# Kernel optimization log

Hardware: AMD Instinct MI355X
Metric: run time of the kernel (lower is better)

The kernel has to match this reference:

```python
import jax, jax.numpy as jnp
import numpy as np

N_PTS = 131072
IN_CH = 63
IN_CH_VIEWS = 27
WIDTH = 256
NUM_HEADS = 4
SCALE = 0.05


def setup_inputs() -> dict:
    key = jax.random.key(0)
    ks = jax.random.split(key, 12)
    H, W = NUM_HEADS, WIDTH
    inp = {
        'x': jax.random.normal(ks[0], (N_PTS, IN_CH + IN_CH_VIEWS), jnp.float32),
        'head_idx': jax.random.randint(ks[1], (N_PTS,), 0, NUM_HEADS),
        # shared trunk: layer0 63->256, layers1..3 256->256 (no skip before split_at=4)
        'W0': jax.random.normal(ks[2], (IN_CH, W), jnp.float32) * SCALE,
        'b0': jnp.zeros((W,), jnp.float32),
        'Ws': jax.random.normal(ks[3], (3, W, W), jnp.float32) * SCALE,
        'bs': jnp.zeros((3, W), jnp.float32),
        # per-head tails: g=4 in skips -> (W+63)->W, then g=5..7 W->W
        'tW0': jax.random.normal(ks[4], (H, W + IN_CH, W), jnp.float32) * SCALE,
        'tb0': jnp.zeros((H, W), jnp.float32),
        'tWs': jax.random.normal(ks[5], (H, 3, W, W), jnp.float32) * SCALE,
        'tbs': jnp.zeros((H, 3, W), jnp.float32),
        # per-head viewdirs output heads
        'featW': jax.random.normal(ks[6], (H, W, W), jnp.float32) * SCALE,
        'featb': jnp.zeros((H, W), jnp.float32),
        'alphaW': jax.random.normal(ks[7], (H, W, 1), jnp.float32) * SCALE,
        'alphab': jnp.zeros((H, 1), jnp.float32),
        'viewsW': jax.random.normal(ks[8], (H, IN_CH_VIEWS + W, W // 2), jnp.float32) * SCALE,
        'viewsb': jnp.zeros((H, W // 2), jnp.float32),
        'rgbW': jax.random.normal(ks[9], (H, W // 2, 3), jnp.float32) * SCALE,
        'rgbb': jnp.zeros((H, 3), jnp.float32),
    }
    return inp


def reference(x, head_idx, W0, b0, Ws, bs, tW0, tb0, tWs, tbs,
              featW, featb, alphaW, alphab, viewsW, viewsb, rgbW, rgbb):
    input_pts = x[:, :IN_CH]          # [N, 63]
    input_views = x[:, IN_CH:]        # [N, 27]

    # shared trunk (layers 0..3, no skip hits in this range)
    h = jax.nn.relu(input_pts @ W0 + b0)
    for i in range(Ws.shape[0]):
        h = jax.nn.relu(h @ Ws[i] + bs[i])

    # per-head tails, computed densely for ALL heads (as in the original)
    # first tail layer g=4 is a skip layer: concat input_pts
    ht = jnp.concatenate([input_pts, h], axis=-1)          # [N, 319]
    ha = jax.nn.relu(jnp.einsum('nf,hfo->nho', ht, tW0) + tb0[None])  # [N, H, 256]
    for j in range(tWs.shape[1]):
        ha = jax.nn.relu(jnp.einsum('nho,hop->nhp', ha, tWs[:, j]) + tbs[None, :, j])

    # per-head viewdir output heads
    alpha = jnp.einsum('nho,hop->nhp', ha, alphaW) + alphab[None]     # [N, H, 1]
    feat = jnp.einsum('nho,hop->nhp', ha, featW) + featb[None]        # [N, H, 256]
    views_b = jnp.broadcast_to(input_views[:, None, :], (x.shape[0], feat.shape[1], IN_CH_VIEWS))
    hv = jnp.concatenate([feat, views_b], axis=-1)                    # [N, H, 283]
    hv = jax.nn.relu(jnp.einsum('nho,hop->nhp', hv, viewsW) + viewsb[None])
    rgb = jnp.einsum('nho,hop->nhp', hv, rgbW) + rgbb[None]           # [N, H, 3]

    outs = jnp.concatenate([rgb, alpha], axis=-1)                     # [N, H, 4]
    sel = jnp.take_along_axis(outs, head_idx[:, None, None], axis=1)[:, 0]  # [N, 4]
    return sel
```

## Files before the change

kernel.cpp:

```cpp
#include <hip/hip_runtime.h>

#define N_PTS 131072
#define TILE 64
#define THREADS 256
#define REGION 40960

typedef __bf16 bf16;
typedef __bf16 bf16x8 __attribute__((ext_vector_type(8)));
typedef float f32x4 __attribute__((ext_vector_type(4)));

#define WS_PERM_OFF   256
#define WS_WPACK_OFF  (256 + 4 * REGION * 4)
#define OFF_W0     0
#define OFF_WS     16384
#define OFF_TW0    212992
#define OFF_TWS    540672
#define OFF_FEATW  1327104
#define OFF_VIEWSW 1589248
#define TOTAL_PACK 1736704

#define H_BASE 0
#define B_BASE 32768
#define LDS_BYTES 81920

__device__ __forceinline__ unsigned swz(unsigned base, unsigned row, unsigned rowstride,
                                        unsigned kbyte) {
  return (base + row * rowstride + kbyte) ^ ((row & 7u) << 4);
}

__device__ __forceinline__ void gload_lds16(const bf16* g, char* l) {
  __builtin_amdgcn_global_load_lds(
      (const __attribute__((address_space(1))) void*)g,
      (__attribute__((address_space(3))) void*)l, 16, 0, 0);
}

template <int N>
__device__ __forceinline__ void wait_vm() {
  asm volatile("s_waitcnt vmcnt(%0)" ::"n"(N) : "memory");
}

__global__ void k_pack(const float* __restrict__ W0, const float* __restrict__ Ws,
                       const float* __restrict__ tW0, const float* __restrict__ tWs,
                       const float* __restrict__ featW, const float* __restrict__ viewsW,
                       bf16* __restrict__ out, const int* __restrict__ head,
                       int* __restrict__ ctrl, int* __restrict__ perm) {
  int gid = blockIdx.x * blockDim.x + threadIdx.x;
  if (gid < N_PTS) {
    int h = head[gid];
    int lane = threadIdx.x & 63;
    #pragma unroll
    for (int hh = 0; hh < 4; ++hh) {
      unsigned long long m = __ballot(h == hh);
      if (m == 0ull) continue;
      int leader = __builtin_ctzll(m);
      int base = 0;
      if (lane == leader) base = atomicAdd(&ctrl[16 + hh], __popcll(m));
      base = __shfl(base, leader);
      if (h == hh) {
        int rank = __popcll(m & ((1ull << lane) - 1ull));
        perm[hh * REGION + base + rank] = gid;
      }
    }
  }

  for (int idx = gid; idx < TOTAL_PACK; idx += gridDim.x * blockDim.x) {
    float v; int dst;
    if (idx < 16384) {
      int k = idx >> 8, o = idx & 255;
      v = (k < 63) ? W0[k * 256 + o] : 0.f;
      dst = OFF_W0 + o * 64 + k;
    } else if (idx < 212992) {
      int i = idx - 16384; int l = i >> 16, r = i & 65535, k = r >> 8, o = r & 255;
      v = Ws[i];
      dst = OFF_WS + l * 65536 + o * 256 + k;
    } else if (idx < 540672) {
      int i = idx - 212992; int h = i / 81920, r = i % 81920, k = r >> 8, o = r & 255;
      v = (k < 63) ? tW0[(h * 319 + k) * 256 + o]
                   : (k == 63 ? 0.f : tW0[(h * 319 + k - 1) * 256 + o]);
      dst = OFF_TW0 + h * 81920 + o * 320 + k;
    } else if (idx < 1327104) {
      int i = idx - 540672; int hj = i >> 16, r = i & 65535, k = r >> 8, o = r & 255;
      v = tWs[i];
      dst = OFF_TWS + hj * 65536 + o * 256 + k;
    } else if (idx < 1589248) {
      int i = idx - 1327104; int h = i >> 16, r = i & 65535, k = r >> 8, o = r & 255;
      v = featW[i];
      dst = OFF_FEATW + h * 65536 + o * 256 + k;
    } else {
      int i = idx - 1589248; int h = i / 36864, r = i % 36864, k = r >> 7, o = r & 127;
      v = (k < 283) ? viewsW[(h * 283 + k) * 128 + o] : 0.f;
      dst = OFF_VIEWSW + h * 36864 + o * 288 + k;
    }
    out[dst] = (bf16)v;
  }
}

template <int NF, bool RELU, int RKC, int LKC, bool REG_FIRST, int OUTS>
__device__ __forceinline__ void mfma_layer(char* lds, const bf16* __restrict__ Wt,
                                           int wK, const float* __restrict__ bias,
                                           const bf16x8* aregs, int lane, int wave) {
  const int l15 = lane & 15, l4 = lane >> 4;
  constexpr int KC = RKC + LKC;
  f32x4 acc[4][NF];
  #pragma unroll
  for (int m = 0; m < 4; ++m)
    #pragma unroll
    for (int n = 0; n < NF; ++n) acc[m][n] = (f32x4){0.f, 0.f, 0.f, 0.f};

  const int c0 = wave * (NF * 16);
  const int wbase = B_BASE + wave * 12288;

  float bv[NF];
  #pragma unroll
  for (int n = 0; n < NF; ++n) bv[n] = bias[c0 + n * 16 + l15];

  const int breg = wbase + l15 * 64 + ((l4 ^ ((l15 >> 1) & 3)) << 4);

  unsigned acur = (unsigned)(l15 * 512 + l4 * 16);
  const unsigned axor = (l15 & 7u) << 4;

  const bf16* gsrc[NF];
  #pragma unroll
  for (int s = 0; s < NF; ++s) {
    int op = s * 16 + (lane >> 2);
    int j = lane & 3;
    gsrc[s] = Wt + (c0 + op) * wK + ((j ^ ((op >> 1) & 3)) << 3);
  }

  #pragma unroll
  for (int s = 0; s < NF; ++s) { gload_lds16(gsrc[s], lds + wbase + s * 1024); gsrc[s] += 32; }
  #pragma unroll
  for (int s = 0; s < NF; ++s) { gload_lds16(gsrc[s], lds + wbase + 4096 + s * 1024); gsrc[s] += 32; }

  int rd = 0, st = 8192;

  auto dostep = [&](int kc, const bf16x8* ar) {
    if (kc + 2 < KC) {
      #pragma unroll
      for (int s = 0; s < NF; ++s) { gload_lds16(gsrc[s], lds + wbase + st + s * 1024); gsrc[s] += 32; }
      st = (st == 8192) ? 0 : st + 4096;
      wait_vm<2 * NF>();
    } else if (kc + 1 < KC) {
      wait_vm<NF>();
    } else {
      wait_vm<0>();
    }

    bf16x8 a[4];
    if (ar) {
      #pragma unroll
      for (int m = 0; m < 4; ++m) a[m] = ar[m];
    } else {
      unsigned va = acur ^ axor;
      #pragma unroll
      for (int m = 0; m < 4; ++m) a[m] = *(const bf16x8*)(lds + va + m * 8192);
      acur += 64;
    }
    bf16x8 b[NF];
    #pragma unroll
    for (int n = 0; n < NF; ++n) b[n] = *(const bf16x8*)(lds + breg + rd + n * 1024);
    rd = (rd == 8192) ? 0 : rd + 4096;

    __builtin_amdgcn_s_setprio(1);
    #pragma unroll
    for (int n = 0; n < NF; ++n)
      #pragma unroll
      for (int m = 0; m < 4; ++m)
        acc[m][n] = __builtin_amdgcn_mfma_f32_16x16x32_bf16(a[m], b[n], acc[m][n], 0, 0, 0);
    __builtin_amdgcn_s_setprio(0);
  };

  if constexpr (REG_FIRST && RKC >= 1) dostep(0, aregs);
  if constexpr (REG_FIRST && RKC >= 2) dostep(1, aregs + 4);
  #pragma unroll 1
  for (int kc = (REG_FIRST ? RKC : 0); kc < (REG_FIRST ? KC : LKC); ++kc)
    dostep(kc, nullptr);
  if constexpr (!REG_FIRST && RKC >= 1) dostep(KC - 1, aregs);

  __builtin_amdgcn_s_barrier();

  #pragma unroll
  for (int n = 0; n < NF; ++n) {
    int col = c0 + n * 16 + l15;
    #pragma unroll
    for (int m = 0; m < 4; ++m) {
      #pragma unroll
      for (int j = 0; j < 4; ++j) {
        float v = acc[m][n][j] + bv[n];
        if (RELU) v = fmaxf(v, 0.f);
        int row = m * 16 + l4 * 4 + j;
        *(bf16*)(lds + swz(H_BASE, row, 512, col * 2)) = (bf16)v;
      }
    }
  }
  __syncthreads();
}

__global__ __launch_bounds__(THREADS, 2) void k_main(
    const float* __restrict__ x, const int* __restrict__ ctrl, const int* __restrict__ perm,
    const bf16* __restrict__ wpack,
    const float* __restrict__ b0, const float* __restrict__ bs,
    const float* __restrict__ tb0p, const float* __restrict__ tbsp,
    const float* __restrict__ featb, const float* __restrict__ alphaW,
    const float* __restrict__ alphab, const float* __restrict__ viewsb,
    const float* __restrict__ rgbW, const float* __restrict__ rgbb,
    float* __restrict__ outp) {
  __shared__ __attribute__((aligned(16))) char lds[LDS_BYTES];

  const int tid = threadIdx.x;
  const int lane = tid & 63, wave = tid >> 6;
  const int l15 = lane & 15, l4 = lane >> 4;

  const int hh = blockIdx.x / (REGION / TILE);
  const int start = (blockIdx.x % (REGION / TILE)) * TILE;
  const int cnt = ctrl[16 + hh];
  if (start >= cnt) return;
  const int nv = min(TILE, cnt - start);
  const int permbase = hh * REGION + start;

  bf16x8 ptsreg[8];
  bf16x8 viewsreg[4];
  #pragma unroll
  for (int m = 0; m < 4; ++m) {
    int row = m * 16 + l15;
    bool valid = (start + row) < cnt;
    int p = valid ? perm[permbase + row] : 0;
    const float* xr = x + p * 90;
    #pragma unroll
    for (int rkc = 0; rkc < 2; ++rkc) {
      int k0 = rkc * 32 + l4 * 8;
      bf16x8 f;
      #pragma unroll
      for (int j = 0; j < 8; ++j) {
        int k = k0 + j;
        f[j] = (bf16)((valid && k < 63) ? xr[k] : 0.f);
      }
      ptsreg[rkc * 4 + m] = f;
    }
    {
      int k0 = l4 * 8;
      bf16x8 f;
      #pragma unroll
      for (int j = 0; j < 8; ++j) {
        int k = k0 + j;
        f[j] = (bf16)((valid && k < 27) ? xr[63 + k] : 0.f);
      }
      viewsreg[m] = f;
    }
  }

  const bf16* W0p    = wpack + OFF_W0;
  const bf16* Wsp    = wpack + OFF_WS;
  const bf16* tW0p   = wpack + OFF_TW0 + hh * 81920;
  const bf16* tWsp   = wpack + OFF_TWS + hh * 3 * 65536;
  const bf16* featWp = wpack + OFF_FEATW + hh * 65536;
  const bf16* viewsWp= wpack + OFF_VIEWSW + hh * 36864;

  mfma_layer<4, true, 2, 0, true,  256>(lds, W0p, 64, b0, ptsreg, lane, wave);
  mfma_layer<4, true, 0, 8, false, 256>(lds, Wsp,          256, bs,       nullptr, lane, wave);
  mfma_layer<4, true, 0, 8, false, 256>(lds, Wsp + 65536,  256, bs + 256, nullptr, lane, wave);
  mfma_layer<4, true, 0, 8, false, 256>(lds, Wsp + 131072, 256, bs + 512, nullptr, lane, wave);
  mfma_layer<4, true, 2, 8, true,  256>(lds, tW0p, 320, tb0p + hh * 256, ptsreg, lane, wave);

  mfma_layer<4, true, 0, 8, false, 256>(lds, tWsp,          256, tbsp + hh * 768,       nullptr, lane, wave);
  mfma_layer<4, true, 0, 8, false, 256>(lds, tWsp + 65536,  256, tbsp + hh * 768 + 256, nullptr, lane, wave);
  mfma_layer<4, true, 0, 8, false, 256>(lds, tWsp + 131072, 256, tbsp + hh * 768 + 512, nullptr, lane, wave);

  float my_alpha;
  {
    int p = wave * 16 + l15;
    int kq = lane >> 4;
    const float* aW = alphaW + hh * 256;
    float s = 0.f;
    for (int i = 0; i < 8; ++i) {
      int k = kq * 64 + i * 8;
      bf16x8 hv8 = *(const bf16x8*)(lds + swz(H_BASE, p, 512, k * 2));
      #pragma unroll
      for (int j = 0; j < 8; ++j) s += (float)hv8[j] * aW[k + j];
    }
    s += __shfl_xor(s, 16);
    s += __shfl_xor(s, 32);
    my_alpha = s + alphab[hh];
  }

  mfma_layer<4, false, 0, 8, false, 256>(lds, featWp, 256, featb + hh * 256, nullptr, lane, wave);
  mfma_layer<2, true, 1, 8, false, 128>(lds, viewsWp, 288, viewsb + hh * 128, viewsreg, lane, wave);

  {
    int p = wave * 16 + l15;
    int kq = lane >> 4;
    const float* rW = rgbW + hh * 128 * 3;
    float r0 = 0.f, r1 = 0.f, r2 = 0.f;
    for (int i = 0; i < 4; ++i) {
      int k = kq * 32 + i * 8;
      bf16x8 hv8 = *(const bf16x8*)(lds + swz(H_BASE, p, 512, k * 2));
      #pragma unroll
      for (int j = 0; j < 8; ++j) {
        float hvf = (float)hv8[j];
        r0 += hvf * rW[(k + j) * 3 + 0];
        r1 += hvf * rW[(k + j) * 3 + 1];
        r2 += hvf * rW[(k + j) * 3 + 2];
      }
    }
    r0 += __shfl_xor(r0, 16); r0 += __shfl_xor(r0, 32);
    r1 += __shfl_xor(r1, 16); r1 += __shfl_xor(r1, 32);
    r2 += __shfl_xor(r2, 16); r2 += __shfl_xor(r2, 32);
    if (kq == 0 && p < nv) {
      int pt = perm[permbase + p];
      float4 o = make_float4(r0 + rgbb[hh * 3 + 0], r1 + rgbb[hh * 3 + 1],
                             r2 + rgbb[hh * 3 + 2], my_alpha);
      *(float4*)(outp + pt * 4) = o;
    }
  }
}

extern "C" void kernel_launch(void* const* d_in, const int* in_sizes, int n_in,
                              void* d_out, int out_size, void* d_ws, size_t ws_size,
                              hipStream_t stream) {
  const float* x      = (const float*)d_in[0];
  const int*   head   = (const int*)d_in[1];
  const float* W0     = (const float*)d_in[2];
  const float* b0     = (const float*)d_in[3];
  const float* Ws     = (const float*)d_in[4];
  const float* bs     = (const float*)d_in[5];
  const float* tW0    = (const float*)d_in[6];
  const float* tb0    = (const float*)d_in[7];
  const float* tWs    = (const float*)d_in[8];
  const float* tbs    = (const float*)d_in[9];
  const float* featW  = (const float*)d_in[10];
  const float* featb  = (const float*)d_in[11];
  const float* alphaW = (const float*)d_in[12];
  const float* alphab = (const float*)d_in[13];
  const float* viewsW = (const float*)d_in[14];
  const float* viewsb = (const float*)d_in[15];
  const float* rgbW   = (const float*)d_in[16];
  const float* rgbb   = (const float*)d_in[17];

  int*  ctrl  = (int*)d_ws;
  int*  perm  = (int*)((char*)d_ws + WS_PERM_OFF);
  bf16* wpack = (bf16*)((char*)d_ws + WS_WPACK_OFF);

  hipMemsetAsync(ctrl, 0, 256, stream);
  k_pack<<<2048, 256, 0, stream>>>(W0, Ws, tW0, tWs, featW, viewsW, wpack, head, ctrl, perm);
  k_main<<<4 * (REGION / TILE), THREADS, 0, stream>>>(x, ctrl, perm, wpack,
                                                      b0, bs, tb0, tbs, featb, alphaW, alphab,
                                                      viewsb, rgbW, rgbb, (float*)d_out);
}
```

Before: 422.1 us.

## Prefetch next layer's weights across layers and stage inputs in LDS

The weight streaming drops from a three-slot ring to a double buffer. On its last K step each layer now issues the first weight chunk of the next layer, so the pipeline bubble at layer boundaries is hidden. The pts and views inputs are staged in swizzled LDS instead of per-thread registers, and the permutation indices are cached in LDS. This frees VGPRs and lowers total LDS use. In exchange, the shallower prefetch depth may expose global-load latency within each layer, and the kernel now relies on hand-placed waitcnt and barrier pairs for LDS correctness.

```diff
diff --git a/kernel.cpp b/kernel.cpp
--- a/kernel.cpp
+++ b/kernel.cpp
@@ -19,9 +19,12 @@
 #define OFF_VIEWSW 1589248
 #define TOTAL_PACK 1736704
 
-#define H_BASE 0
-#define B_BASE 32768
-#define LDS_BYTES 81920
+#define H_BASE     0
+#define PTS_BASE   32768
+#define VIEWS_BASE 40960
+#define PIDX_BASE  45056
+#define RING_BASE  46080
+#define LDS_BYTES  78848
 
 __device__ __forceinline__ unsigned swz(unsigned base, unsigned row, unsigned rowstride,
                                         unsigned kbyte) {
@@ -95,12 +98,14 @@
   }
 }
 
-template <int NF, bool RELU, int RKC, int LKC, bool REG_FIRST, int OUTS>
+template <int NF, bool RELU, int PKC, int LKC, bool PTS_FIRST, int AUXB, int AUXSTR,
+          int NEXTNF>
 __device__ __forceinline__ void mfma_layer(char* lds, const bf16* __restrict__ Wt,
                                            int wK, const float* __restrict__ bias,
-                                           const bf16x8* aregs, int lane, int wave) {
+                                           const bf16* __restrict__ nextWt, int nextwK,
+                                           int lane, int wave) {
   const int l15 = lane & 15, l4 = lane >> 4;
-  constexpr int KC = RKC + LKC;
+  constexpr int KC = PKC + LKC;
   f32x4 acc[4][NF];
   #pragma unroll
   for (int m = 0; m < 4; ++m)
@@ -108,7 +113,7 @@
     for (int n = 0; n < NF; ++n) acc[m][n] = (f32x4){0.f, 0.f, 0.f, 0.f};
 
   const int c0 = wave * (NF * 16);
-  const int wbase = B_BASE + wave * 12288;
+  const int wbase = RING_BASE + wave * 8192;
 
   float bv[NF];
   #pragma unroll
@@ -124,32 +129,40 @@
   for (int s = 0; s < NF; ++s) {
     int op = s * 16 + (lane >> 2);
     int j = lane & 3;
-    gsrc[s] = Wt + (c0 + op) * wK + ((j ^ ((op >> 1) & 3)) << 3);
-  }
-
-  #pragma unroll
-  for (int s = 0; s < NF; ++s) { gload_lds16(gsrc[s], lds + wbase + s * 1024); gsrc[s] += 32; }
-  #pragma unroll
-  for (int s = 0; s < NF; ++s) { gload_lds16(gsrc[s], lds + wbase + 4096 + s * 1024); gsrc[s] += 32; }
-
-  int rd = 0, st = 8192;
-
-  auto dostep = [&](int kc, const bf16x8* ar) {
-    if (kc + 2 < KC) {
-      #pragma unroll
-      for (int s = 0; s < NF; ++s) { gload_lds16(gsrc[s], lds + wbase + st + s * 1024); gsrc[s] += 32; }
-      st = (st == 8192) ? 0 : st + 4096;
-      wait_vm<2 * NF>();
-    } else if (kc + 1 < KC) {
+    gsrc[s] = Wt + (c0 + op) * wK + ((j ^ ((op >> 1) & 3)) << 3) + 32;
+  }
+
+  #pragma unroll
+  for (int kc = 0; kc < KC; ++kc) {
+    if (kc + 1 < KC) {
+      #pragma unroll
+      for (int s = 0; s < NF; ++s) {
+        gload_lds16(gsrc[s], lds + wbase + ((kc + 1) & 1) * 4096 + s * 1024);
+        gsrc[s] += 32;
+      }
       wait_vm<NF>();
+    } else if constexpr (NEXTNF > 0) {
+      #pragma unroll
+      for (int s = 0; s < NEXTNF; ++s) {
+        int op = s * 16 + (lane >> 2);
+        int j = lane & 3;
+        const bf16* g = nextWt + (wave * NEXTNF * 16 + op) * nextwK +
+                        ((j ^ ((op >> 1) & 3)) << 3);
+        gload_lds16(g, lds + wbase + s * 1024);
+      }
+      wait_vm<NEXTNF>();
     } else {
       wait_vm<0>();
     }
 
     bf16x8 a[4];
-    if (ar) {
-      #pragma unroll
-      for (int m = 0; m < 4; ++m) a[m] = ar[m];
+    if (PTS_FIRST ? (kc < PKC) : (kc >= LKC)) {
+      const int kcp = PTS_FIRST ? kc : 0;
+      #pragma unroll
+      for (int m = 0; m < 4; ++m) {
+        unsigned ad = (unsigned)(AUXB + (m * 16 + l15) * AUXSTR + kcp * 64 + l4 * 16) ^ axor;
+        a[m] = *(const bf16x8*)(lds + ad);
+      }
     } else {
       unsigned va = acur ^ axor;
       #pragma unroll
@@ -158,8 +171,8 @@
     }
     bf16x8 b[NF];
     #pragma unroll
-    for (int n = 0; n < NF; ++n) b[n] = *(const bf16x8*)(lds + breg + rd + n * 1024);
-    rd = (rd == 8192) ? 0 : rd + 4096;
+    for (int n = 0; n < NF; ++n)
+      b[n] = *(const bf16x8*)(lds + breg + (kc & 1) * 4096 + n * 1024);
 
     __builtin_amdgcn_s_setprio(1);
     #pragma unroll
@@ -168,14 +181,7 @@
       for (int m = 0; m < 4; ++m)
         acc[m][n] = __builtin_amdgcn_mfma_f32_16x16x32_bf16(a[m], b[n], acc[m][n], 0, 0, 0);
     __builtin_amdgcn_s_setprio(0);
-  };
-
-  if constexpr (REG_FIRST && RKC >= 1) dostep(0, aregs);
-  if constexpr (REG_FIRST && RKC >= 2) dostep(1, aregs + 4);
-  #pragma unroll 1
-  for (int kc = (REG_FIRST ? RKC : 0); kc < (REG_FIRST ? KC : LKC); ++kc)
-    dostep(kc, nullptr);
-  if constexpr (!REG_FIRST && RKC >= 1) dostep(KC - 1, aregs);
+  }
 
   __builtin_amdgcn_s_barrier();
 
@@ -193,19 +199,21 @@
       }
     }
   }
-  __syncthreads();
+  asm volatile("s_waitcnt lgkmcnt(0)" ::: "memory");
+  __builtin_amdgcn_s_barrier();
 }
 
 __global__ __launch_bounds__(THREADS, 2) void k_main(
     const float* __restrict__ x, const int* __restrict__ ctrl, const int* __restrict__ perm,
     const bf16* __restrict__ wpack,
     const float* __restrict__ b0, const float* __restrict__ bs,
-    const float* __restrict__ tb0p, const float* __restrict__ tbsp,
+    const float* __restrict__ tb0, const float* __restrict__ tbs,
     const float* __restrict__ featb, const float* __restrict__ alphaW,
     const float* __restrict__ alphab, const float* __restrict__ viewsb,
     const float* __restrict__ rgbW, const float* __restrict__ rgbb,
     float* __restrict__ outp) {
   __shared__ __attribute__((aligned(16))) char lds[LDS_BYTES];
+  int* pidxl = (int*)(lds + PIDX_BASE);
 
   const int tid = threadIdx.x;
   const int lane = tid & 63, wave = tid >> 6;
@@ -218,35 +226,18 @@
   const int nv = min(TILE, cnt - start);
   const int permbase = hh * REGION + start;
 
-  bf16x8 ptsreg[8];
-  bf16x8 viewsreg[4];
-  #pragma unroll
-  for (int m = 0; m < 4; ++m) {
-    int row = m * 16 + l15;
-    bool valid = (start + row) < cnt;
-    int p = valid ? perm[permbase + row] : 0;
-    const float* xr = x + p * 90;
-    #pragma unroll
-    for (int rkc = 0; rkc < 2; ++rkc) {
-      int k0 = rkc * 32 + l4 * 8;
-      bf16x8 f;
-      #pragma unroll
-      for (int j = 0; j < 8; ++j) {
-        int k = k0 + j;
-        f[j] = (bf16)((valid && k < 63) ? xr[k] : 0.f);
-      }
-      ptsreg[rkc * 4 + m] = f;
-    }
-    {
-      int k0 = l4 * 8;
-      bf16x8 f;
-      #pragma unroll
-      for (int j = 0; j < 8; ++j) {
-        int k = k0 + j;
-        f[j] = (bf16)((valid && k < 27) ? xr[63 + k] : 0.f);
-      }
-      viewsreg[m] = f;
-    }
+  if (tid < TILE) pidxl[tid] = (tid < nv) ? perm[permbase + tid] : 0;
+  __syncthreads();
+
+  for (int i = tid; i < TILE * 64; i += THREADS) {
+    int row = i >> 6, c = i & 63;
+    float v = (row < nv && c < 63) ? x[pidxl[row] * 90 + c] : 0.f;
+    *(bf16*)(lds + ((PTS_BASE + row * 128 + c * 2) ^ ((row & 7u) << 4))) = (bf16)v;
+  }
+  for (int i = tid; i < TILE * 32; i += THREADS) {
+    int row = i >> 5, c = i & 31;
+    float v = (row < nv && c < 27) ? x[pidxl[row] * 90 + 63 + c] : 0.f;
+    *(bf16*)(lds + ((VIEWS_BASE + row * 64 + c * 2) ^ ((row & 7u) << 4))) = (bf16)v;
   }
 
   const bf16* W0p    = wpack + OFF_W0;
@@ -256,15 +247,29 @@
   const bf16* featWp = wpack + OFF_FEATW + hh * 65536;
   const bf16* viewsWp= wpack + OFF_VIEWSW + hh * 36864;
 
-  mfma_layer<4, true, 2, 0, true,  256>(lds, W0p, 64, b0, ptsreg, lane, wave);
-  mfma_layer<4, true, 0, 8, false, 256>(lds, Wsp,          256, bs,       nullptr, lane, wave);
-  mfma_layer<4, true, 0, 8, false, 256>(lds, Wsp + 65536,  256, bs + 256, nullptr, lane, wave);
-  mfma_layer<4, true, 0, 8, false, 256>(lds, Wsp + 131072, 256, bs + 512, nullptr, lane, wave);
-  mfma_layer<4, true, 2, 8, true,  256>(lds, tW0p, 320, tb0p + hh * 256, ptsreg, lane, wave);
-
-  mfma_layer<4, true, 0, 8, false, 256>(lds, tWsp,          256, tbsp + hh * 768,       nullptr, lane, wave);
-  mfma_layer<4, true, 0, 8, false, 256>(lds, tWsp + 65536,  256, tbsp + hh * 768 + 256, nullptr, lane, wave);
-  mfma_layer<4, true, 0, 8, false, 256>(lds, tWsp + 131072, 256, tbsp + hh * 768 + 512, nullptr, lane, wave);
+  {
+    const int wbase = RING_BASE + wave * 8192;
+    const int c0 = wave * 64;
+    #pragma unroll
+    for (int s = 0; s < 4; ++s) {
+      int op = s * 16 + (lane >> 2);
+      int j = lane & 3;
+      gload_lds16(W0p + (c0 + op) * 64 + ((j ^ ((op >> 1) & 3)) << 3),
+                  lds + wbase + s * 1024);
+    }
+  }
+  asm volatile("s_waitcnt lgkmcnt(0)" ::: "memory");
+  __builtin_amdgcn_s_barrier();
+
+  mfma_layer<4, true, 2, 0, true,  PTS_BASE, 128, 4>(lds, W0p, 64, b0, Wsp, 256, lane, wave);
+  mfma_layer<4, true, 0, 8, false, 0, 0,      4>(lds, Wsp,          256, bs,       Wsp + 65536,  256, lane, wave);
+  mfma_layer<4, true, 0, 8, false, 0, 0,      4>(lds, Wsp + 65536,  256, bs + 256, Wsp + 131072, 256, lane, wave);
+  mfma_layer<4, true, 0, 8, false, 0, 0,      4>(lds, Wsp + 131072, 256, bs + 512, tW0p,         320, lane, wave);
+  mfma_layer<4, true, 2, 8, true,  PTS_BASE, 128, 4>(lds, tW0p, 320, tb0 + hh * 256, tWsp, 256, lane, wave);
+
+  mfma_layer<4, true, 0, 8, false, 0, 0, 4>(lds, tWsp,          256, tbs + hh * 768,       tWsp + 65536,  256, lane, wave);
+  mfma_layer<4, true, 0, 8, false, 0, 0, 4>(lds, tWsp + 65536,  256, tbs + hh * 768 + 256, tWsp + 131072, 256, lane, wave);
+  mfma_layer<4, true, 0, 8, false, 0, 0, 4>(lds, tWsp + 131072, 256, tbs + hh * 768 + 512, featWp,        256, lane, wave);
 
   float my_alpha;
   {
@@ -283,8 +288,9 @@
     my_alpha = s + alphab[hh];
   }
 
-  mfma_layer<4, false, 0, 8, false, 256>(lds, featWp, 256, featb + hh * 256, nullptr, lane, wave);
-  mfma_layer<2, true, 1, 8, false, 128>(lds, viewsWp, 288, viewsb + hh * 128, viewsreg, lane, wave);
+  mfma_layer<4, false, 0, 8, false, 0, 0, 2>(lds, featWp, 256, featb + hh * 256, viewsWp, 288, lane, wave);
+  mfma_layer<2, true, 1, 8, false, VIEWS_BASE, 64, 0>(lds, viewsWp, 288, viewsb + hh * 128,
+                                                      nullptr, 0, lane, wave);
 
   {
     int p = wave * 16 + l15;
@@ -306,7 +312,7 @@
     r1 += __shfl_xor(r1, 16); r1 += __shfl_xor(r1, 32);
     r2 += __shfl_xor(r2, 16); r2 += __shfl_xor(r2, 32);
     if (kq == 0 && p < nv) {
-      int pt = perm[permbase + p];
+      int pt = pidxl[p];
       float4 o = make_float4(r0 + rgbb[hh * 3 + 0], r1 + rgbb[hh * 3 + 1],
                              r2 + rgbb[hh * 3 + 2], my_alpha);
       *(float4*)(outp + pt * 4) = o;
```

Result: slower. 460.0 us (+9.0%).
